# Kernel tuning notes

Measured on AMD Instinct MI355X. Metric: run time of the kernel, lower is better.

The kernel has to match this reference:

```python
import jax, jax.numpy as jnp
from jax import lax
import numpy as np
import math

IN_CH = 256
SCALES = [128, 256, 512]
ASPECT = [0.5, 1.0, 2.0]
NUM_A = len(SCALES) * len(ASPECT)  # 9
PRENMS_TOPK = 2000
RPN_TOPK = 1000
NMS_TH = 0.7
MIN_SIZE = 16.0
IMG_H = IMG_W = 1600
FEAT_H = FEAT_W = 200
BBOX_CLIP = math.log(1000.0 / 16.0)  # standard dw/dh clamp in box decoding


def setup_inputs() -> dict:
    key = jax.random.key(0)
    ks = jax.random.split(key, 6)
    image = jax.random.normal(ks[0], (1, 3, IMG_H, IMG_W), jnp.float32)
    feat = jax.random.normal(ks[1], (1, IN_CH, FEAT_H, FEAT_W), jnp.float32)
    # params init per init_weights(): normal(std=0.01), zero bias
    conv_w = jax.random.normal(ks[2], (IN_CH, IN_CH, 3, 3), jnp.float32) * 0.01
    conv_b = jnp.zeros((IN_CH,), jnp.float32)
    cls_w = jax.random.normal(ks[3], (NUM_A, IN_CH, 1, 1), jnp.float32) * 0.01
    cls_b = jnp.zeros((NUM_A,), jnp.float32)
    reg_w = jax.random.normal(ks[4], (NUM_A * 4, IN_CH, 1, 1), jnp.float32) * 0.01
    reg_b = jnp.zeros((NUM_A * 4,), jnp.float32)
    return dict(image=image, feat=feat, conv_w=conv_w, conv_b=conv_b,
                cls_w=cls_w, cls_b=cls_b, reg_w=reg_w, reg_b=reg_b)


def _conv(x, w, b, pad):
    y = lax.conv_general_dilated(x, w, (1, 1), [(pad, pad), (pad, pad)],
                                 dimension_numbers=('NCHW', 'OIHW', 'NCHW'))
    return y + b[None, :, None, None]


def _generate_anchors(img_hw, feat_hw):
    # static (numpy) anchor grid, faithful to generate_anchors_
    gh, gw = feat_hw
    ih, iw = img_hw
    sh, sw = ih // gh, iw // gw
    scales = np.array(SCALES, np.float32)
    ar = np.array(ASPECT, np.float32)
    hr = np.sqrt(ar)
    wr = 1.0 / hr
    ws = (wr[:, None] * scales[None, :]).reshape(-1)
    hs = (hr[:, None] * scales[None, :]).reshape(-1)
    base = np.round(np.stack([-ws, -hs, ws, hs], axis=1) / 2.0)  # (A,4)
    sx = np.arange(gw, dtype=np.float32) * sw
    sy = np.arange(gh, dtype=np.float32) * sh
    yy, xx = np.meshgrid(sy, sx, indexing='ij')
    xx = xx.reshape(-1)
    yy = yy.reshape(-1)
    shifts = np.stack([xx, yy, xx, yy], axis=1)  # (H*W,4)
    anchors = (shifts[:, None, :] + base[None, :, :]).reshape(-1, 4)
    return jnp.asarray(anchors, jnp.float32)


def _apply_deltas(anchors, deltas):
    w = anchors[:, 2] - anchors[:, 0]
    h = anchors[:, 3] - anchors[:, 1]
    cx = anchors[:, 0] + 0.5 * w
    cy = anchors[:, 1] + 0.5 * h
    dx, dy = deltas[:, 0], deltas[:, 1]
    dw = jnp.minimum(deltas[:, 2], BBOX_CLIP)
    dh = jnp.minimum(deltas[:, 3], BBOX_CLIP)
    pcx = dx * w + cx
    pcy = dy * h + cy
    pw = jnp.exp(dw) * w
    ph = jnp.exp(dh) * h
    return jnp.stack([pcx - 0.5 * pw, pcy - 0.5 * ph,
                      pcx + 0.5 * pw, pcy + 0.5 * ph], axis=1)


def _nms_keep(boxes, valid, thresh):
    # boxes sorted by descending score; greedy NMS via dense IoU matrix
    K = boxes.shape[0]
    area = (boxes[:, 2] - boxes[:, 0]) * (boxes[:, 3] - boxes[:, 1])
    lt = jnp.maximum(boxes[:, None, :2], boxes[None, :, :2])
    rb = jnp.minimum(boxes[:, None, 2:], boxes[None, :, 2:])
    wh = jnp.maximum(rb - lt, 0.0)
    inter = wh[..., 0] * wh[..., 1]
    iou = inter / (area[:, None] + area[None, :] - inter + 1e-9)
    idx = jnp.arange(K)

    def body(i, keep):
        sup = (iou[i] > thresh) & keep[i] & (idx > i)
        return keep & (~sup)

    return lax.fori_loop(0, K, body, valid)


def reference(image, feat, conv_w, conv_b, cls_w, cls_b, reg_w, reg_b):
    H, W = feat.shape[-2], feat.shape[-1]
    x = jax.nn.relu(_conv(feat, conv_w, conv_b, 1))          # (1,C,H,W)
    cls = _conv(x, cls_w, cls_b, 0)                          # (1,A,H,W)
    scores = cls.transpose(0, 2, 3, 1).reshape(-1)           # (H*W*A,)
    reg = _conv(x, reg_w, reg_b, 0)                          # (1,4A,H,W)
    deltas = reg.reshape(1, NUM_A, 4, H, W).transpose(0, 3, 4, 1, 2).reshape(-1, 4)
    anchors = _generate_anchors((image.shape[-2], image.shape[-1]), (H, W))
    proposals = _apply_deltas(anchors, lax.stop_gradient(deltas))  # .detach() in source

    s = jax.nn.sigmoid(scores)
    topv, topi = lax.top_k(s, PRENMS_TOPK)                   # sorted descending
    p = proposals[topi]
    ih = jnp.float32(image.shape[-2])
    iw = jnp.float32(image.shape[-1])
    p = jnp.stack([jnp.clip(p[:, 0], 0.0, iw), jnp.clip(p[:, 1], 0.0, ih),
                   jnp.clip(p[:, 2], 0.0, iw), jnp.clip(p[:, 3], 0.0, ih)], axis=1)
    valid = ((p[:, 2] - p[:, 0]) >= MIN_SIZE) & ((p[:, 3] - p[:, 1]) >= MIN_SIZE)
    sc = jnp.where(valid, topv, -1.0)                        # invalid -> score -1 (masked out)
    order = jnp.argsort(-sc)
    b = p[order]
    sc = sc[order]
    v = valid[order]
    keep = _nms_keep(b, v, NMS_TH)
    final = jnp.where(keep, sc, -1.0)
    fi = jnp.argsort(-final)[:RPN_TOPK]                      # post-NMS sort + topk
    sel = final[fi]
    out_boxes = jnp.where(sel[:, None] > 0.0, b[fi], 0.0)
    out_scores = jnp.where(sel > 0.0, sel, 0.0)
    return out_boxes, out_scores
```

## Files before the change

### kernel.cpp

```cpp
#include <hip/hip_runtime.h>
#include <math.h>

#define FH 200
#define FW 200
#define HW 40000
#define NUM_A 9
#define NANCH 360000
#define PRE_K 2000
#define OUT_K 1000
#define IMG_SZ 1600.0f
#define MIN_SZ 16.0f
#define NMS_TH 0.7f
#define BBOX_CLIP_F 4.135166556742356f

#define OFF_HIST   ((size_t)0)
#define OFF_STATE  ((size_t)1024)
#define OFF_CAND   ((size_t)1088)
#define OFF_BOXS   ((size_t)33856)
#define OFF_SCS    ((size_t)65856)
#define OFF_MASK   ((size_t)73856)
#define OFF_DIAG   ((size_t)585856)
#define OFF_AWH    ((size_t)602240)
#define OFF_AWM    ((size_t)1781888)
#define OFF_AWL    ((size_t)2961536)
#define OFF_HWH    ((size_t)4141184)
#define OFF_HWM    ((size_t)4165760)
#define OFF_HWL    ((size_t)4190336)
#define OFF_LOGIT  ((size_t)4214912)
#define OFF_PH     ((size_t)18614912)
#define OFF_PM     ((size_t)39094912)
#define OFF_PL     ((size_t)59574912)
#define OFF_PROP   ((size_t)18614912)
#define OFF_SCORE  ((size_t)24374912)

typedef __attribute__((ext_vector_type(8))) short short8;
typedef __attribute__((ext_vector_type(4))) float floatx4;
#define MFMA16(a, b, c) __builtin_amdgcn_mfma_f32_16x16x32_bf16(a, b, c, 0, 0, 0)

__device__ __forceinline__ unsigned short rne_bf16(float v) {
  unsigned int bb = __float_as_uint(v);
  return (unsigned short)((bb + 0x7FFFu + ((bb >> 16) & 1u)) >> 16);
}

__device__ __forceinline__ void split3(float v, unsigned short& h,
                                       unsigned short& m, unsigned short& l) {
  h = rne_bf16(v);
  float r1 = v - __uint_as_float(((unsigned int)h) << 16);
  m = rne_bf16(r1);
  float r2 = r1 - __uint_as_float(((unsigned int)m) << 16);
  l = rne_bf16(r2);
}

__global__ __launch_bounds__(256) void prep_all(
    const float* __restrict__ feat, const float* __restrict__ w,
    const float* __restrict__ cls_w, const float* __restrict__ reg_w,
    unsigned short* __restrict__ Ph, unsigned short* __restrict__ Pm,
    unsigned short* __restrict__ Pl, uint4* __restrict__ AW_h,
    uint4* __restrict__ AW_m, uint4* __restrict__ AW_l,
    uint4* __restrict__ HwF_h, uint4* __restrict__ HwF_m,
    uint4* __restrict__ HwF_l) {
  int bx = blockIdx.x;
  int t = threadIdx.x;
  if (bx < 1256) {
    int cib = bx & 7;
    int px = (bx >> 3) * 256 + t;
    if (px >= HW) return;
    unsigned short h[32], m[32], l[32];
#pragma unroll
    for (int ci = 0; ci < 32; ++ci)
      split3(feat[(size_t)(cib * 32 + ci) * HW + px], h[ci], m[ci], l[ci]);
    size_t base = ((size_t)cib * HW + px) * 32;
    uint4* dh = (uint4*)(Ph + base);
    uint4* dm = (uint4*)(Pm + base);
    uint4* dl = (uint4*)(Pl + base);
#pragma unroll
    for (int k = 0; k < 4; ++k) {
      uint4 vh, vm, vl;
      vh.x = h[k * 8 + 0] | (h[k * 8 + 1] << 16);
      vh.y = h[k * 8 + 2] | (h[k * 8 + 3] << 16);
      vh.z = h[k * 8 + 4] | (h[k * 8 + 5] << 16);
      vh.w = h[k * 8 + 6] | (h[k * 8 + 7] << 16);
      vm.x = m[k * 8 + 0] | (m[k * 8 + 1] << 16);
      vm.y = m[k * 8 + 2] | (m[k * 8 + 3] << 16);
      vm.z = m[k * 8 + 4] | (m[k * 8 + 5] << 16);
      vm.w = m[k * 8 + 6] | (m[k * 8 + 7] << 16);
      vl.x = l[k * 8 + 0] | (l[k * 8 + 1] << 16);
      vl.y = l[k * 8 + 2] | (l[k * 8 + 3] << 16);
      vl.z = l[k * 8 + 4] | (l[k * 8 + 5] << 16);
      vl.w = l[k * 8 + 6] | (l[k * 8 + 7] << 16);
      dh[k] = vh; dm[k] = vm; dl[k] = vl;
    }
    return;
  }
  int gid = (bx - 1256) * 256 + t;
  unsigned short h[8], m[8], l[8];
  if (gid < 73728) {
    int L = gid & 63;
    int idx = gid >> 6;
    int cib = idx & 7;
    int tmp = idx >> 3;
    int tap = tmp % 9;
    int ctg = tmp / 9;
    int co = ctg * 16 + (L & 15);
    int ci0 = cib * 32 + (L >> 4) * 8;
#pragma unroll
    for (int j = 0; j < 8; ++j)
      split3(w[(size_t)co * 2304 + (ci0 + j) * 9 + tap], h[j], m[j], l[j]);
    uint4 vh, vm, vl;
    vh.x = h[0] | (h[1] << 16); vh.y = h[2] | (h[3] << 16);
    vh.z = h[4] | (h[5] << 16); vh.w = h[6] | (h[7] << 16);
    vm.x = m[0] | (m[1] << 16); vm.y = m[2] | (m[3] << 16);
    vm.z = m[4] | (m[5] << 16); vm.w = m[6] | (m[7] << 16);
    vl.x = l[0] | (l[1] << 16); vl.y = l[2] | (l[3] << 16);
    vl.z = l[4] | (l[5] << 16); vl.w = l[6] | (l[7] << 16);
    AW_h[gid] = vh; AW_m[gid] = vm; AW_l[gid] = vl;
  } else if (gid < 73728 + 1536) {
    int g2 = gid - 73728;
    int L = g2 & 63;
    int idx = g2 >> 6;
    int kb = idx & 7;
    int mt = idx >> 3;
    int mm = mt * 16 + (L & 15);
    int co0 = kb * 32 + (L >> 4) * 8;
#pragma unroll
    for (int j = 0; j < 8; ++j) {
      float v = 0.f;
      if (mm < 9) v = cls_w[mm * 256 + co0 + j];
      else if (mm < 45) v = reg_w[(mm - 9) * 256 + co0 + j];
      split3(v, h[j], m[j], l[j]);
    }
    uint4 vh, vm, vl;
    vh.x = h[0] | (h[1] << 16); vh.y = h[2] | (h[3] << 16);
    vh.z = h[4] | (h[5] << 16); vh.w = h[6] | (h[7] << 16);
    vm.x = m[0] | (m[1] << 16); vm.y = m[2] | (m[3] << 16);
    vm.z = m[4] | (m[5] << 16); vm.w = m[6] | (m[7] << 16);
    vl.x = l[0] | (l[1] << 16); vl.y = l[2] | (l[3] << 16);
    vl.z = l[4] | (l[5] << 16); vl.w = l[6] | (l[7] << 16);
    HwF_h[g2] = vh; HwF_m[g2] = vm; HwF_l[g2] = vl;
  }
}

__global__ __launch_bounds__(256, 3) void conv_mfma(
    const unsigned short* __restrict__ Ph, const unsigned short* __restrict__ Pm,
    const unsigned short* __restrict__ Pl, const uint4* __restrict__ AW_h,
    const uint4* __restrict__ AW_m, const uint4* __restrict__ AW_l,
    const uint4* __restrict__ HwF_h, const uint4* __restrict__ HwF_m,
    const uint4* __restrict__ HwF_l, const float* __restrict__ bias,
    float* __restrict__ logits) {
  __shared__ alignas(16) unsigned short smem[26112];
  const int t = threadIdx.x;
  const int L = t & 63, wv = t >> 6;
  const int q = L >> 4, nl = L & 15;
  const int w0 = blockIdx.x * 16;
  const int h0 = blockIdx.y * 8;
  const int cb = blockIdx.z;

  floatx4 acc[2][8];
#pragma unroll
  for (int ct = 0; ct < 2; ++ct)
#pragma unroll
    for (int r = 0; r < 8; ++r) acc[ct][r] = (floatx4)0.f;

  unsigned short* flh = smem;
  unsigned short* flm = smem + 7200;
  unsigned short* fll = smem + 14400;

  for (int cib = 0; cib < 8; ++cib) {
    __syncthreads();
#pragma unroll
    for (int j = 0; j < 9; ++j) {
      const int p = j / 3;
      const int c = (j % 3) * 256 + t;
      if (c < 720) {
        int rr = (int)((unsigned)c / 72u);
        int rem = c - rr * 72;
        int cc = rem >> 2, q16 = rem & 3;
        int gr = h0 - 1 + rr, gc = w0 - 1 + cc;
        uint4 v; v.x = v.y = v.z = v.w = 0u;
        if ((unsigned)gr < (unsigned)FH && (unsigned)gc < (unsigned)FW) {
          const unsigned short* pp = (p == 0) ? Ph : (p == 1) ? Pm : Pl;
          v = *(const uint4*)(pp +
                ((size_t)(cib * HW + gr * FW + gc) * 32 + q16 * 8));
        }
        *(uint4*)(smem + p * 7200 + rr * 720 + cc * 40 + q16 * 8) = v;
      }
    }
    __syncthreads();
    __builtin_amdgcn_s_setprio(1);
    const int ctg0 = cb * 8 + wv * 2;
    for (int kh = 0; kh < 3; ++kh) {
      for (int kw = 0; kw < 3; ++kw) {
        const int tap = kh * 3 + kw;
        const int abase = ((ctg0 * 9 + tap) * 8 + cib) * 64 + L;
        const int abase1 = abase + 9 * 8 * 64;
        short8 ah0 = ((const short8*)AW_h)[abase];
        short8 am0 = ((const short8*)AW_m)[abase];
        short8 al0 = ((const short8*)AW_l)[abase];
        short8 ah1 = ((const short8*)AW_h)[abase1];
        short8 am1 = ((const short8*)AW_m)[abase1];
        short8 al1 = ((const short8*)AW_l)[abase1];
        const int cbase = (nl + kw) * 40 + q * 8;
#pragma unroll
        for (int r = 0; r < 8; ++r) {
          const int off = (r + kh) * 720 + cbase;
          short8 bh = *(const short8*)(flh + off);
          short8 bm = *(const short8*)(flm + off);
          short8 bl = *(const short8*)(fll + off);
          acc[0][r] = MFMA16(ah0, bh, acc[0][r]);
          acc[0][r] = MFMA16(ah0, bm, acc[0][r]);
          acc[0][r] = MFMA16(am0, bh, acc[0][r]);
          acc[0][r] = MFMA16(ah0, bl, acc[0][r]);
          acc[0][r] = MFMA16(am0, bm, acc[0][r]);
          acc[0][r] = MFMA16(al0, bh, acc[0][r]);
          acc[1][r] = MFMA16(ah1, bh, acc[1][r]);
          acc[1][r] = MFMA16(ah1, bm, acc[1][r]);
          acc[1][r] = MFMA16(am1, bh, acc[1][r]);
          acc[1][r] = MFMA16(ah1, bl, acc[1][r]);
          acc[1][r] = MFMA16(am1, bm, acc[1][r]);
          acc[1][r] = MFMA16(al1, bh, acc[1][r]);
        }
      }
    }
    __builtin_amdgcn_s_setprio(0);
  }

  float bv[2][4];
#pragma unroll
  for (int ct = 0; ct < 2; ++ct)
#pragma unroll
    for (int i = 0; i < 4; ++i)
      bv[ct][i] = bias[cb * 128 + (wv * 2 + ct) * 16 + q * 4 + i];

  unsigned short* xlh = smem;
  unsigned short* xlm = smem + 8704;
  unsigned short* xll = smem + 17408;

  for (int hp = 0; hp < 2; ++hp) {
    __syncthreads();
#pragma unroll
    for (int ct = 0; ct < 2; ++ct) {
#pragma unroll
      for (int rr = 0; rr < 4; ++rr) {
        int r = hp * 4 + rr;
        unsigned short xh[4], xm[4], xl_[4];
#pragma unroll
        for (int i = 0; i < 4; ++i) {
          float xv = fmaxf(acc[ct][r][i] + bv[ct][i], 0.f);
          split3(xv, xh[i], xm[i], xl_[i]);
        }
        int px_l = rr * 16 + nl;
        int co_l = (wv * 2 + ct) * 16 + q * 4;
        uint2 ph, pm, pl;
        ph.x = xh[0] | (xh[1] << 16); ph.y = xh[2] | (xh[3] << 16);
        pm.x = xm[0] | (xm[1] << 16); pm.y = xm[2] | (xm[3] << 16);
        pl.x = xl_[0] | (xl_[1] << 16); pl.y = xl_[2] | (xl_[3] << 16);
        *(uint2*)(xlh + px_l * 136 + co_l) = ph;
        *(uint2*)(xlm + px_l * 136 + co_l) = pm;
        *(uint2*)(xll + px_l * 136 + co_l) = pl;
      }
    }
    __syncthreads();
    floatx4 ha[3];
#pragma unroll
    for (int mt = 0; mt < 3; ++mt) ha[mt] = (floatx4)0.f;
    for (int ks = 0; ks < 4; ++ks) {
      const int off = (wv * 16 + nl) * 136 + ks * 32 + q * 8;
      short8 bh = *(const short8*)(xlh + off);
      short8 bm = *(const short8*)(xlm + off);
      short8 bl = *(const short8*)(xll + off);
#pragma unroll
      for (int mt = 0; mt < 3; ++mt) {
        const int hb = (mt * 8 + cb * 4 + ks) * 64 + L;
        short8 hh = ((const short8*)HwF_h)[hb];
        short8 hm = ((const short8*)HwF_m)[hb];
        short8 hl = ((const short8*)HwF_l)[hb];
        ha[mt] = MFMA16(hh, bh, ha[mt]);
        ha[mt] = MFMA16(hh, bm, ha[mt]);
        ha[mt] = MFMA16(hm, bh, ha[mt]);
        ha[mt] = MFMA16(hh, bl, ha[mt]);
        ha[mt] = MFMA16(hm, bm, ha[mt]);
        ha[mt] = MFMA16(hl, bh, ha[mt]);
      }
    }
    int gr = h0 + hp * 4 + wv;
    int gc = w0 + nl;
    if (gc < FW) {
      float* lp = logits + ((size_t)cb * HW + (size_t)(gr * FW + gc)) * 45;
#pragma unroll
      for (int mt = 0; mt < 3; ++mt)
#pragma unroll
        for (int i = 0; i < 4; ++i) {
          int head = mt * 16 + q * 4 + i;
          if (head < 45) lp[head] = ha[mt][i];
        }
    }
  }
}

__global__ __launch_bounds__(256) void finalize_kernel(
    const float* __restrict__ logits, const float* __restrict__ cls_b,
    const float* __restrict__ reg_b, float* __restrict__ prop,
    float* __restrict__ score, unsigned int* __restrict__ hist,
    unsigned int* __restrict__ state) {
  __shared__ unsigned int hsh[256], s1[256];
  __shared__ int lastb;
  int t = threadIdx.x;
  hsh[t] = 0u;
  __syncthreads();
  int px = blockIdx.x * 256 + t;
  if (px < HW) {
    float A[45];
    const float* lpA = logits + (size_t)px * 45;
    const float* lpB = logits + (size_t)HW * 45 + (size_t)px * 45;
#pragma unroll
    for (int i = 0; i < 45; ++i) A[i] = lpA[i] + lpB[i];
    const float scv[3] = {128.f, 256.f, 512.f};
    const float arv[3] = {0.5f, 1.f, 2.f};
    float sx = (float)(px % FW) * 8.0f;
    float sy = (float)(px / FW) * 8.0f;
#pragma unroll
    for (int a = 0; a < NUM_A; ++a) {
      int ai = a / 3, si = a % 3;
      float hr = sqrtf(arv[ai]);
      float wr = 1.0f / hr;
      float rw = nearbyintf(wr * scv[si] * 0.5f);
      float rh = nearbyintf(hr * scv[si] * 0.5f);
      float ax0 = sx - rw, ay0 = sy - rh, ax1 = sx + rw, ay1 = sy + rh;
      float aw = ax1 - ax0, ah = ay1 - ay0;
      float cx = ax0 + 0.5f * aw, cy = ay0 + 0.5f * ah;
      float dx = A[9 + a * 4 + 0] + reg_b[a * 4 + 0];
      float dy = A[9 + a * 4 + 1] + reg_b[a * 4 + 1];
      float dw = fminf(A[9 + a * 4 + 2] + reg_b[a * 4 + 2], BBOX_CLIP_F);
      float dh = fminf(A[9 + a * 4 + 3] + reg_b[a * 4 + 3], BBOX_CLIP_F);
      float pcx = dx * aw + cx;
      float pcy = dy * ah + cy;
      float pw = expf(dw) * aw;
      float ph = expf(dh) * ah;
      size_t base = (size_t)(px * NUM_A + a) * 4;
      prop[base + 0] = pcx - 0.5f * pw;
      prop[base + 1] = pcy - 0.5f * ph;
      prop[base + 2] = pcx + 0.5f * pw;
      prop[base + 3] = pcy + 0.5f * ph;
      float lg = A[a] + cls_b[a];
      float sv = 1.0f / (1.0f + expf(-lg));
      score[px * NUM_A + a] = sv;
      atomicAdd(&hsh[__float_as_uint(sv) >> 24], 1u);
    }
  }
  __syncthreads();
  if (hsh[t]) atomicAdd(&hist[t], hsh[t]);
  __syncthreads();
  if (t == 0) lastb = (atomicAdd(&state[8], 1u) == gridDim.x - 1u) ? 1 : 0;
  __syncthreads();
  if (!lastb) return;
  __threadfence();
  unsigned int hv = hist[t];
  hist[t] = 0u;
  hsh[t] = hv;
  __syncthreads();
  unsigned int* A = hsh;
  unsigned int* B = s1;
  for (int off = 1; off < 256; off <<= 1) {
    B[t] = A[t] + ((t + off < 256) ? A[t + off] : 0u);
    __syncthreads();
    unsigned int* tmp = A; A = B; B = tmp;
  }
  unsigned int rem = (unsigned)PRE_K;
  unsigned int suf = A[t];
  unsigned int sufn = (t < 255) ? A[t + 1] : 0u;
  if (suf >= rem && sufn < rem) {
    state[0] = (unsigned int)t;
    state[1] = rem - sufn;
  }
}

__global__ __launch_bounds__(256) void hist_scan_kernel(
    const float* __restrict__ score, unsigned int* __restrict__ hist,
    unsigned int* __restrict__ state, unsigned int* __restrict__ ticket,
    int pass) {
  __shared__ unsigned int h[256], s1[256];
  __shared__ int lastb;
  int t = threadIdx.x;
  h[t] = 0;
  __syncthreads();
  unsigned int prefix = state[0];
  int shift = 24 - 8 * pass;
  for (int i = blockIdx.x * 256 + t; i < NANCH; i += gridDim.x * 256) {
    unsigned int key = __float_as_uint(score[i]);
    if ((key >> (32 - 8 * pass)) == prefix)
      atomicAdd(&h[(key >> shift) & 255u], 1u);
  }
  __syncthreads();
  if (h[t]) atomicAdd(&hist[t], h[t]);
  __syncthreads();
  if (t == 0) lastb = (atomicAdd(ticket, 1u) == gridDim.x - 1u) ? 1 : 0;
  __syncthreads();
  if (!lastb) return;
  __threadfence();
  unsigned int hv = hist[t];
  hist[t] = 0u;
  h[t] = hv;
  __syncthreads();
  unsigned int* A = h;
  unsigned int* B = s1;
  for (int off = 1; off < 256; off <<= 1) {
    B[t] = A[t] + ((t + off < 256) ? A[t + off] : 0u);
    __syncthreads();
    unsigned int* tmp = A; A = B; B = tmp;
  }
  unsigned int rem = state[1];
  unsigned int suf = A[t];
  unsigned int sufn = (t < 255) ? A[t + 1] : 0u;
  if (suf >= rem && sufn < rem) {
    state[0] = (prefix << 8) | (unsigned int)t;
    state[1] = rem - sufn;
  }
}

__global__ __launch_bounds__(256) void collect_kernel(
    const float* __restrict__ score, unsigned int* __restrict__ state,
    unsigned long long* __restrict__ cand) {
  unsigned int T = state[0] << 8;
  for (int i = blockIdx.x * 256 + threadIdx.x; i < NANCH; i += gridDim.x * 256) {
    unsigned int key = __float_as_uint(score[i]);
    if (key >= T) {
      unsigned int pos = atomicAdd(&state[4], 1u);
      if (pos < 4096u)
        cand[pos] = ((unsigned long long)key << 32) |
                    (unsigned long long)(~(unsigned int)i);
    }
  }
}

__global__ __launch_bounds__(1024) void sort_gather(
    const unsigned long long* __restrict__ cand,
    const unsigned int* __restrict__ state, const float* __restrict__ prop,
    const float* __restrict__ score, float* __restrict__ boxes_s,
    float* __restrict__ sc_s) {
  __shared__ unsigned long long sk[4096];
  int t = threadIdx.x;
  unsigned int cnt = state[4];
  if (cnt > 4096u) cnt = 4096u;
  for (int e = t; e < 4096; e += 1024) sk[e] = (e < (int)cnt) ? cand[e] : 0ull;
  __syncthreads();
  const int n = (cnt <= 2048u) ? 2048 : 4096;
  for (int k = 2; k <= n; k <<= 1) {
    for (int j = k >> 1; j > 0; j >>= 1) {
      for (int i = t; i < n; i += 1024) {
        int l = i ^ j;
        if (l > i) {
          unsigned long long a = sk[i], bb = sk[l];
          bool up = ((i & k) == 0);
          bool sw = up ? (a < bb) : (a > bb);
          if (sw) { sk[i] = bb; sk[l] = a; }
        }
      }
      __syncthreads();
    }
  }
  float bx[2][4];
  float sc2[2] = {-1.f, -1.f};
  bool valid2[2] = {false, false};
#pragma unroll
  for (int s = 0; s < 2; ++s) {
    int i = t + s * 1024;
    bx[s][0] = bx[s][1] = bx[s][2] = bx[s][3] = 0.f;
    if (i < PRE_K) {
      unsigned long long v = sk[i];
      unsigned int idx = ~(unsigned int)(v & 0xFFFFFFFFull);
      float4 p = *(const float4*)(prop + (size_t)idx * 4);
      float x0 = fminf(fmaxf(p.x, 0.f), IMG_SZ);
      float y0 = fminf(fmaxf(p.y, 0.f), IMG_SZ);
      float x1 = fminf(fmaxf(p.z, 0.f), IMG_SZ);
      float y1 = fminf(fmaxf(p.w, 0.f), IMG_SZ);
      bool valid = (x1 - x0 >= MIN_SZ) && (y1 - y0 >= MIN_SZ);
      bx[s][0] = x0; bx[s][1] = y0; bx[s][2] = x1; bx[s][3] = y1;
      valid2[s] = valid;
      sc2[s] = valid ? score[idx] : -1.0f;
    }
  }
  __syncthreads();
  int* A = (int*)sk;
  int* B = A + 2048;
#pragma unroll
  for (int s = 0; s < 2; ++s) {
    int i = t + s * 1024;
    A[i] = (i < PRE_K && valid2[s]) ? 1 : 0;
  }
  __syncthreads();
  for (int off = 1; off < 2048; off <<= 1) {
#pragma unroll
    for (int s = 0; s < 2; ++s) {
      int i = t + s * 1024;
      B[i] = A[i] + ((i >= off) ? A[i - off] : 0);
    }
    __syncthreads();
    int* tmp = A; A = B; B = tmp;
  }
  int total = A[2047];
#pragma unroll
  for (int s = 0; s < 2; ++s) {
    int i = t + s * 1024;
    if (i < PRE_K) {
      int inc = A[i];
      int pos = valid2[s] ? (inc - 1) : (total + (i - inc));
      boxes_s[pos * 4 + 0] = bx[s][0];
      boxes_s[pos * 4 + 1] = bx[s][1];
      boxes_s[pos * 4 + 2] = bx[s][2];
      boxes_s[pos * 4 + 3] = bx[s][3];
      sc_s[pos] = sc2[s];
    }
  }
}

__global__ __launch_bounds__(256) void iou_kernel(
    const float* __restrict__ boxes_s, unsigned long long* __restrict__ mask,
    unsigned long long* __restrict__ diag) {
  __shared__ float4 cbw[4][64];
  const int t = threadIdx.x;
  const int wvi = t >> 6, lane = t & 63;
  const int bj = blockIdx.x * 4 + wvi;
  const int bi = blockIdx.y;
  {
    int jc = bj * 64 + lane;
    float4 z; z.x = z.y = z.z = z.w = 0.f;
    cbw[wvi][lane] = (jc < PRE_K) ? *(const float4*)(boxes_s + (size_t)jc * 4) : z;
  }
  __syncthreads();
  int i = bi * 64 + lane;
  if (i >= PRE_K) return;
  float4 a = *(const float4*)(boxes_s + (size_t)i * 4);
  float areaA = (a.z - a.x) * (a.w - a.y);
  unsigned long long bits = 0ull;
  for (int jj = 0; jj < 64; ++jj) {
    int j = bj * 64 + jj;
    if (j < PRE_K && j > i) {
      float4 b = cbw[wvi][jj];
      float areaB = (b.z - b.x) * (b.w - b.y);
      float ltx = fmaxf(a.x, b.x), lty = fmaxf(a.y, b.y);
      float rbx = fminf(a.z, b.z), rby = fminf(a.w, b.w);
      float w = fmaxf(rbx - ltx, 0.f), h = fmaxf(rby - lty, 0.f);
      float inter = w * h;
      float iou = inter / (areaA + areaB - inter + 1e-9f);
      if (iou > NMS_TH) bits |= (1ull << jj);
    }
  }
  mask[(size_t)i * 32 + bj] = bits;
  if (bi == bj) diag[i] = bits;
}

__global__ __launch_bounds__(256) void nms_out_kernel(
    const float* __restrict__ boxes_s, const float* __restrict__ sc_s,
    const unsigned long long* __restrict__ mask,
    const unsigned long long* __restrict__ diag, float* __restrict__ out) {
  int t = threadIdx.x;
  for (int e = t; e < (OUT_K * 4 + OUT_K); e += 256) out[e] = 0.f;
  __shared__ unsigned long long keepw[32];
  if (t < 64) {
    unsigned long long removed = 0ull;
    if (t < 32) {
      keepw[t] = 0ull;
#pragma unroll
      for (int k = 0; k < 64; ++k) {
        int idx = t * 64 + k;
        if (idx >= PRE_K || sc_s[idx] < 0.f) removed |= (1ull << k);
      }
    }
    const int w = t & 31;
    const int half = t >> 5;
    unsigned int kept = 0;
    for (int b = 0; b < 32; ++b) {
      unsigned long long d = diag[b * 64 + t];
      unsigned long long dead = __shfl(removed, b);
      unsigned long long alive = 0ull;
#pragma unroll
      for (int k = 0; k < 64; ++k) {
        unsigned long long dk = __shfl(d, k);
        if (!((dead >> k) & 1ull)) {
          alive |= (1ull << k);
          dead |= dk;
        }
      }
      if (t == 0) keepw[b] = alive;
      kept += (unsigned)__popcll(alive);
      if (kept >= (unsigned)OUT_K || b == 31) break;
      unsigned long long am = alive;
      const long long rb = (long long)b * 64;
      while (am) {
        int k0 = __ffsll(am) - 1; am &= am - 1;
        int k1 = k0, k2 = k0, k3 = k0, k4 = k0, k5 = k0, k6 = k0, k7 = k0;
        int k8 = k0, k9 = k0, k10 = k0, k11 = k0, k12 = k0, k13 = k0;
        int k14 = k0, k15 = k0;
        if (am) { k1 = __ffsll(am) - 1; am &= am - 1; }
        if (am) { k2 = __ffsll(am) - 1; am &= am - 1; }
        if (am) { k3 = __ffsll(am) - 1; am &= am - 1; }
        if (am) { k4 = __ffsll(am) - 1; am &= am - 1; }
        if (am) { k5 = __ffsll(am) - 1; am &= am - 1; }
        if (am) { k6 = __ffsll(am) - 1; am &= am - 1; }
        if (am) { k7 = __ffsll(am) - 1; am &= am - 1; }
        if (am) { k8 = __ffsll(am) - 1; am &= am - 1; }
        if (am) { k9 = __ffsll(am) - 1; am &= am - 1; }
        if (am) { k10 = __ffsll(am) - 1; am &= am - 1; }
        if (am) { k11 = __ffsll(am) - 1; am &= am - 1; }
        if (am) { k12 = __ffsll(am) - 1; am &= am - 1; }
        if (am) { k13 = __ffsll(am) - 1; am &= am - 1; }
        if (am) { k14 = __ffsll(am) - 1; am &= am - 1; }
        if (am) { k15 = __ffsll(am) - 1; am &= am - 1; }
        unsigned long long v0 = mask[(size_t)(rb + (half ? k1 : k0)) * 32 + w];
        unsigned long long v1 = mask[(size_t)(rb + (half ? k3 : k2)) * 32 + w];
        unsigned long long v2 = mask[(size_t)(rb + (half ? k5 : k4)) * 32 + w];
        unsigned long long v3 = mask[(size_t)(rb + (half ? k7 : k6)) * 32 + w];
        unsigned long long v4 = mask[(size_t)(rb + (half ? k9 : k8)) * 32 + w];
        unsigned long long v5 = mask[(size_t)(rb + (half ? k11 : k10)) * 32 + w];
        unsigned long long v6 = mask[(size_t)(rb + (half ? k13 : k12)) * 32 + w];
        unsigned long long v7 = mask[(size_t)(rb + (half ? k15 : k14)) * 32 + w];
        unsigned long long vv = v0 | v1 | v2 | v3 | v4 | v5 | v6 | v7;
        unsigned long long hv = __shfl(vv, w + 32);
        if (t < 32) removed |= vv | hv;
      }
    }
  }
  __syncthreads();
  __shared__ unsigned int wbase[32];
  if (t == 0) {
    unsigned int s = 0;
    for (int k = 0; k < 32; ++k) {
      wbase[k] = s;
      s += (unsigned)__popcll(keepw[k]);
    }
  }
  __syncthreads();
  for (int i = t; i < PRE_K; i += 256) {
    unsigned long long w2 = keepw[i >> 6];
    if ((w2 >> (i & 63)) & 1ull) {
      unsigned int pos =
          wbase[i >> 6] +
          (unsigned)__popcll(w2 & ((1ull << (i & 63)) - 1ull));
      if (pos < OUT_K) {
        out[pos * 4 + 0] = boxes_s[i * 4 + 0];
        out[pos * 4 + 1] = boxes_s[i * 4 + 1];
        out[pos * 4 + 2] = boxes_s[i * 4 + 2];
        out[pos * 4 + 3] = boxes_s[i * 4 + 3];
        out[OUT_K * 4 + pos] = sc_s[i];
      }
    }
  }
}

extern "C" void kernel_launch(void* const* d_in, const int* in_sizes, int n_in,
                              void* d_out, int out_size, void* d_ws,
                              size_t ws_size, hipStream_t stream) {
  const float* feat = (const float*)d_in[1];
  const float* convw = (const float*)d_in[2];
  const float* convb = (const float*)d_in[3];
  const float* clsw = (const float*)d_in[4];
  const float* clsb = (const float*)d_in[5];
  const float* regw = (const float*)d_in[6];
  const float* regb = (const float*)d_in[7];

  char* ws = (char*)d_ws;
  unsigned int* hist = (unsigned int*)(ws + OFF_HIST);
  unsigned int* state = (unsigned int*)(ws + OFF_STATE);
  unsigned long long* cand = (unsigned long long*)(ws + OFF_CAND);
  float* boxes_s = (float*)(ws + OFF_BOXS);
  float* sc_s = (float*)(ws + OFF_SCS);
  unsigned long long* mask = (unsigned long long*)(ws + OFF_MASK);
  unsigned long long* diag = (unsigned long long*)(ws + OFF_DIAG);
  uint4* AW_h = (uint4*)(ws + OFF_AWH);
  uint4* AW_m = (uint4*)(ws + OFF_AWM);
  uint4* AW_l = (uint4*)(ws + OFF_AWL);
  uint4* HwF_h = (uint4*)(ws + OFF_HWH);
  uint4* HwF_m = (uint4*)(ws + OFF_HWM);
  uint4* HwF_l = (uint4*)(ws + OFF_HWL);
  float* logits = (float*)(ws + OFF_LOGIT);
  unsigned short* Ph = (unsigned short*)(ws + OFF_PH);
  unsigned short* Pm = (unsigned short*)(ws + OFF_PM);
  unsigned short* Pl = (unsigned short*)(ws + OFF_PL);
  float* prop = (float*)(ws + OFF_PROP);
  float* score = (float*)(ws + OFF_SCORE);
  float* out = (float*)d_out;

  hipMemsetAsync(ws, 0, OFF_STATE + 64, stream);

  prep_all<<<1550, 256, 0, stream>>>(feat, convw, clsw, regw, Ph, Pm, Pl,
                                     AW_h, AW_m, AW_l, HwF_h, HwF_m, HwF_l);
  conv_mfma<<<dim3(13, 25, 2), 256, 0, stream>>>(Ph, Pm, Pl, AW_h, AW_m, AW_l,
                                                 HwF_h, HwF_m, HwF_l, convb,
                                                 logits);
  finalize_kernel<<<157, 256, 0, stream>>>(logits, clsb, regb, prop, score,
                                           hist, state);
  for (int p = 1; p < 3; ++p)
    hist_scan_kernel<<<256, 256, 0, stream>>>(score, hist, state,
                                              &state[8 + p], p);
  collect_kernel<<<256, 256, 0, stream>>>(score, state, cand);
  sort_gather<<<1, 1024, 0, stream>>>(cand, state, prop, score, boxes_s, sc_s);
  iou_kernel<<<dim3(8, 32), 256, 0, stream>>>(boxes_s, mask, diag);
  nms_out_kernel<<<1, 256, 0, stream>>>(boxes_s, sc_s, mask, diag, out);
}
```

Measured before the change: 553.3 us.

## Replace single-block bitonic sort with parallel rank sort and fuse IoU with NMS

```diff
diff --git a/kernel.cpp b/kernel.cpp
--- a/kernel.cpp
+++ b/kernel.cpp
@@ -32,6 +32,9 @@
 #define OFF_PL     ((size_t)59574912)
 #define OFF_PROP   ((size_t)18614912)
 #define OFF_SCORE  ((size_t)24374912)
+#define OFF_BT     ((size_t)25817088)
+#define OFF_ST     ((size_t)25849088)
+#define OFF_VT     ((size_t)25857088)
 
 typedef __attribute__((ext_vector_type(8))) short short8;
 typedef __attribute__((ext_vector_type(4))) float floatx4;
@@ -58,9 +61,13 @@
     unsigned short* __restrict__ Pl, uint4* __restrict__ AW_h,
     uint4* __restrict__ AW_m, uint4* __restrict__ AW_l,
     uint4* __restrict__ HwF_h, uint4* __restrict__ HwF_m,
-    uint4* __restrict__ HwF_l) {
+    uint4* __restrict__ HwF_l, unsigned int* __restrict__ zeroreg) {
   int bx = blockIdx.x;
   int t = threadIdx.x;
+  if (bx == 0) {
+    zeroreg[t] = 0u;
+    if (t < 16) zeroreg[256 + t] = 0u;
+  }
   if (bx < 1256) {
     int cib = bx & 7;
     int px = (bx >> 3) * 256 + t;
@@ -432,62 +439,59 @@
   }
 }
 
-__global__ __launch_bounds__(1024) void sort_gather(
+__global__ __launch_bounds__(128) void rank_gather(
     const unsigned long long* __restrict__ cand,
     const unsigned int* __restrict__ state, const float* __restrict__ prop,
-    const float* __restrict__ score, float* __restrict__ boxes_s,
-    float* __restrict__ sc_s) {
-  __shared__ unsigned long long sk[4096];
-  int t = threadIdx.x;
+    const float* __restrict__ score, float* __restrict__ btmp,
+    float* __restrict__ stmp, int* __restrict__ vtmp) {
+  __shared__ unsigned long long tile[128];
+  const int t = threadIdx.x;
+  const int i = blockIdx.x * 128 + t;
   unsigned int cnt = state[4];
   if (cnt > 4096u) cnt = 4096u;
-  for (int e = t; e < 4096; e += 1024) sk[e] = (e < (int)cnt) ? cand[e] : 0ull;
-  __syncthreads();
-  const int n = (cnt <= 2048u) ? 2048 : 4096;
-  for (int k = 2; k <= n; k <<= 1) {
-    for (int j = k >> 1; j > 0; j >>= 1) {
-      for (int i = t; i < n; i += 1024) {
-        int l = i ^ j;
-        if (l > i) {
-          unsigned long long a = sk[i], bb = sk[l];
-          bool up = ((i & k) == 0);
-          bool sw = up ? (a < bb) : (a > bb);
-          if (sw) { sk[i] = bb; sk[l] = a; }
-        }
-      }
-      __syncthreads();
-    }
-  }
-  float bx[2][4];
-  float sc2[2] = {-1.f, -1.f};
-  bool valid2[2] = {false, false};
+  unsigned long long my = (i < (int)cnt) ? cand[i] : 0ull;
+  int rank = 0;
+  for (unsigned int base = 0; base < cnt; base += 128u) {
+    __syncthreads();
+    if (base + t < cnt) tile[t] = cand[base + t];
+    __syncthreads();
+    unsigned int lim = cnt - base;
+    if (lim > 128u) lim = 128u;
+    for (unsigned int j = 0; j < lim; ++j)
+      rank += (tile[j] > my) ? 1 : 0;
+  }
+  if (i >= (int)cnt || rank >= PRE_K) return;
+  unsigned int idx = ~(unsigned int)(my & 0xFFFFFFFFull);
+  float4 p = *(const float4*)(prop + (size_t)idx * 4);
+  float x0 = fminf(fmaxf(p.x, 0.f), IMG_SZ);
+  float y0 = fminf(fmaxf(p.y, 0.f), IMG_SZ);
+  float x1 = fminf(fmaxf(p.z, 0.f), IMG_SZ);
+  float y1 = fminf(fmaxf(p.w, 0.f), IMG_SZ);
+  bool valid = (x1 - x0 >= MIN_SZ) && (y1 - y0 >= MIN_SZ);
+  btmp[rank * 4 + 0] = x0;
+  btmp[rank * 4 + 1] = y0;
+  btmp[rank * 4 + 2] = x1;
+  btmp[rank * 4 + 3] = y1;
+  vtmp[rank] = valid ? 1 : 0;
+  stmp[rank] = valid ? score[idx] : -1.0f;
+}
+
+__global__ __launch_bounds__(1024) void part_kernel(
+    const float* __restrict__ btmp, const float* __restrict__ stmp,
+    const int* __restrict__ vtmp, float* __restrict__ boxes_s,
+    float* __restrict__ sc_s) {
+  __shared__ int s0[2048], s1[2048];
+  int t = threadIdx.x;
+  int v2[2];
 #pragma unroll
   for (int s = 0; s < 2; ++s) {
     int i = t + s * 1024;
-    bx[s][0] = bx[s][1] = bx[s][2] = bx[s][3] = 0.f;
-    if (i < PRE_K) {
-      unsigned long long v = sk[i];
-      unsigned int idx = ~(unsigned int)(v & 0xFFFFFFFFull);
-      float4 p = *(const float4*)(prop + (size_t)idx * 4);
-      float x0 = fminf(fmaxf(p.x, 0.f), IMG_SZ);
-      float y0 = fminf(fmaxf(p.y, 0.f), IMG_SZ);
-      float x1 = fminf(fmaxf(p.z, 0.f), IMG_SZ);
-      float y1 = fminf(fmaxf(p.w, 0.f), IMG_SZ);
-      bool valid = (x1 - x0 >= MIN_SZ) && (y1 - y0 >= MIN_SZ);
-      bx[s][0] = x0; bx[s][1] = y0; bx[s][2] = x1; bx[s][3] = y1;
-      valid2[s] = valid;
-      sc2[s] = valid ? score[idx] : -1.0f;
-    }
-  }
-  __syncthreads();
-  int* A = (int*)sk;
-  int* B = A + 2048;
-#pragma unroll
-  for (int s = 0; s < 2; ++s) {
-    int i = t + s * 1024;
-    A[i] = (i < PRE_K && valid2[s]) ? 1 : 0;
-  }
-  __syncthreads();
+    v2[s] = (i < PRE_K) ? vtmp[i] : 0;
+    s0[i] = v2[s];
+  }
+  __syncthreads();
+  int* A = s0;
+  int* B = s1;
   for (int off = 1; off < 2048; off <<= 1) {
 #pragma unroll
     for (int s = 0; s < 2; ++s) {
@@ -503,20 +507,25 @@
     int i = t + s * 1024;
     if (i < PRE_K) {
       int inc = A[i];
-      int pos = valid2[s] ? (inc - 1) : (total + (i - inc));
-      boxes_s[pos * 4 + 0] = bx[s][0];
-      boxes_s[pos * 4 + 1] = bx[s][1];
-      boxes_s[pos * 4 + 2] = bx[s][2];
-      boxes_s[pos * 4 + 3] = bx[s][3];
-      sc_s[pos] = sc2[s];
-    }
-  }
-}
-
-__global__ __launch_bounds__(256) void iou_kernel(
-    const float* __restrict__ boxes_s, unsigned long long* __restrict__ mask,
-    unsigned long long* __restrict__ diag) {
+      int pos = v2[s] ? (inc - 1) : (total + (i - inc));
+      boxes_s[pos * 4 + 0] = btmp[i * 4 + 0];
+      boxes_s[pos * 4 + 1] = btmp[i * 4 + 1];
+      boxes_s[pos * 4 + 2] = btmp[i * 4 + 2];
+      boxes_s[pos * 4 + 3] = btmp[i * 4 + 3];
+      sc_s[pos] = stmp[i];
+    }
+  }
+}
+
+__global__ __launch_bounds__(256) void iou_nms(
+    const float* __restrict__ boxes_s, const float* __restrict__ sc_s,
+    unsigned long long* __restrict__ mask,
+    unsigned long long* __restrict__ diag, unsigned int* __restrict__ done,
+    float* __restrict__ out) {
   __shared__ float4 cbw[4][64];
+  __shared__ int lastflag;
+  __shared__ unsigned long long keepw[32];
+  __shared__ unsigned int wbase[32];
   const int t = threadIdx.x;
   const int wvi = t >> 6, lane = t & 63;
   const int bj = blockIdx.x * 4 + wvi;
@@ -528,34 +537,35 @@
   }
   __syncthreads();
   int i = bi * 64 + lane;
-  if (i >= PRE_K) return;
-  float4 a = *(const float4*)(boxes_s + (size_t)i * 4);
-  float areaA = (a.z - a.x) * (a.w - a.y);
-  unsigned long long bits = 0ull;
-  for (int jj = 0; jj < 64; ++jj) {
-    int j = bj * 64 + jj;
-    if (j < PRE_K && j > i) {
-      float4 b = cbw[wvi][jj];
-      float areaB = (b.z - b.x) * (b.w - b.y);
-      float ltx = fmaxf(a.x, b.x), lty = fmaxf(a.y, b.y);
-      float rbx = fminf(a.z, b.z), rby = fminf(a.w, b.w);
-      float w = fmaxf(rbx - ltx, 0.f), h = fmaxf(rby - lty, 0.f);
-      float inter = w * h;
-      float iou = inter / (areaA + areaB - inter + 1e-9f);
-      if (iou > NMS_TH) bits |= (1ull << jj);
-    }
-  }
-  mask[(size_t)i * 32 + bj] = bits;
-  if (bi == bj) diag[i] = bits;
-}
-
-__global__ __launch_bounds__(256) void nms_out_kernel(
-    const float* __restrict__ boxes_s, const float* __restrict__ sc_s,
-    const unsigned long long* __restrict__ mask,
-    const unsigned long long* __restrict__ diag, float* __restrict__ out) {
-  int t = threadIdx.x;
+  if (i < PRE_K) {
+    float4 a = *(const float4*)(boxes_s + (size_t)i * 4);
+    float areaA = (a.z - a.x) * (a.w - a.y);
+    unsigned long long bits = 0ull;
+    for (int jj = 0; jj < 64; ++jj) {
+      int j = bj * 64 + jj;
+      if (j < PRE_K && j > i) {
+        float4 b = cbw[wvi][jj];
+        float areaB = (b.z - b.x) * (b.w - b.y);
+        float ltx = fmaxf(a.x, b.x), lty = fmaxf(a.y, b.y);
+        float rbx = fminf(a.z, b.z), rby = fminf(a.w, b.w);
+        float w = fmaxf(rbx - ltx, 0.f), h = fmaxf(rby - lty, 0.f);
+        float inter = w * h;
+        float iou = inter / (areaA + areaB - inter + 1e-9f);
+        if (iou > NMS_TH) bits |= (1ull << jj);
+      }
+    }
+    mask[(size_t)i * 32 + bj] = bits;
+    if (bi == bj) diag[i] = bits;
+  }
+  __syncthreads();
+  if (t == 0) {
+    __threadfence();
+    lastflag = (atomicAdd(done, 1u) == gridDim.x * gridDim.y - 1u) ? 1 : 0;
+  }
+  __syncthreads();
+  if (!lastflag) return;
+  __threadfence();
   for (int e = t; e < (OUT_K * 4 + OUT_K); e += 256) out[e] = 0.f;
-  __shared__ unsigned long long keepw[32];
   if (t < 64) {
     unsigned long long removed = 0ull;
     if (t < 32) {
@@ -621,7 +631,6 @@
     }
   }
   __syncthreads();
-  __shared__ unsigned int wbase[32];
   if (t == 0) {
     unsigned int s = 0;
     for (int k = 0; k < 32; ++k) {
@@ -630,18 +639,18 @@
     }
   }
   __syncthreads();
-  for (int i = t; i < PRE_K; i += 256) {
-    unsigned long long w2 = keepw[i >> 6];
-    if ((w2 >> (i & 63)) & 1ull) {
+  for (int i2 = t; i2 < PRE_K; i2 += 256) {
+    unsigned long long w2 = keepw[i2 >> 6];
+    if ((w2 >> (i2 & 63)) & 1ull) {
       unsigned int pos =
-          wbase[i >> 6] +
-          (unsigned)__popcll(w2 & ((1ull << (i & 63)) - 1ull));
+          wbase[i2 >> 6] +
+          (unsigned)__popcll(w2 & ((1ull << (i2 & 63)) - 1ull));
       if (pos < OUT_K) {
-        out[pos * 4 + 0] = boxes_s[i * 4 + 0];
-        out[pos * 4 + 1] = boxes_s[i * 4 + 1];
-        out[pos * 4 + 2] = boxes_s[i * 4 + 2];
-        out[pos * 4 + 3] = boxes_s[i * 4 + 3];
-        out[OUT_K * 4 + pos] = sc_s[i];
+        out[pos * 4 + 0] = boxes_s[i2 * 4 + 0];
+        out[pos * 4 + 1] = boxes_s[i2 * 4 + 1];
+        out[pos * 4 + 2] = boxes_s[i2 * 4 + 2];
+        out[pos * 4 + 3] = boxes_s[i2 * 4 + 3];
+        out[OUT_K * 4 + pos] = sc_s[i2];
       }
     }
   }
@@ -678,12 +687,14 @@
   unsigned short* Pl = (unsigned short*)(ws + OFF_PL);
   float* prop = (float*)(ws + OFF_PROP);
   float* score = (float*)(ws + OFF_SCORE);
+  float* btmp = (float*)(ws + OFF_BT);
+  float* stmp = (float*)(ws + OFF_ST);
+  int* vtmp = (int*)(ws + OFF_VT);
   float* out = (float*)d_out;
 
-  hipMemsetAsync(ws, 0, OFF_STATE + 64, stream);
-
   prep_all<<<1550, 256, 0, stream>>>(feat, convw, clsw, regw, Ph, Pm, Pl,
-                                     AW_h, AW_m, AW_l, HwF_h, HwF_m, HwF_l);
+                                     AW_h, AW_m, AW_l, HwF_h, HwF_m, HwF_l,
+                                     hist);
   conv_mfma<<<dim3(13, 25, 2), 256, 0, stream>>>(Ph, Pm, Pl, AW_h, AW_m, AW_l,
                                                  HwF_h, HwF_m, HwF_l, convb,
                                                  logits);
@@ -693,7 +704,9 @@
     hist_scan_kernel<<<256, 256, 0, stream>>>(score, hist, state,
                                               &state[8 + p], p);
   collect_kernel<<<256, 256, 0, stream>>>(score, state, cand);
-  sort_gather<<<1, 1024, 0, stream>>>(cand, state, prop, score, boxes_s, sc_s);
-  iou_kernel<<<dim3(8, 32), 256, 0, stream>>>(boxes_s, mask, diag);
-  nms_out_kernel<<<1, 256, 0, stream>>>(boxes_s, sc_s, mask, diag, out);
-}
+  rank_gather<<<32, 128, 0, stream>>>(cand, state, prop, score, btmp, stmp,
+                                      vtmp);
+  part_kernel<<<1, 1024, 0, stream>>>(btmp, stmp, vtmp, boxes_s, sc_s);
+  iou_nms<<<dim3(8, 32), 256, 0, stream>>>(boxes_s, sc_s, mask, diag,
+                                           &state[12], out);
+}
```

Result: no change. 557.7 us (+0.8%).
